# Optimization experiments

Measured on AMD Instinct MI355X. Metric: run time of the kernel, lower is better.

## Reference

```python
import jax, jax.numpy as jnp
import numpy as np

H = 16  # n_heads

def _split_heads(x, n_heads):
    B, S, Dm = x.shape
    return x.reshape(B, S, n_heads, Dm // n_heads).transpose(0, 2, 1, 3)  # [B,H,S,D]

def _matmul_prefix_sum(x, y, z):
    """Faithful, efficient form of the TF matmul_prefix_sum.
    TF builds yz[s] = y[s] (x) z[s] outer products, cumsums over s, then
    contracts with x[t]/ (t+1).  That equals a causal-masked bilinear form:
      out[t, j] = (1/(t+1)) * sum_{s<=t} (x[t]. y[s]) * z[s, j]
    so we compute (x y^T * tril / idx) @ z without the 5D intermediate.
    """
    S = x.shape[2]
    idx = jnp.arange(1, S + 1, dtype=x.dtype)[:, None]        # position 1..S
    mask = jnp.tril(jnp.ones((S, S), dtype=x.dtype))
    scores = jnp.einsum('bhtd,bhsd->bhts', x, y) * (mask / idx)
    return jnp.einsum('bhts,bhsj->bhtj', scores, z)

def setup_inputs() -> dict:
    key = jax.random.key(0)
    ks = jax.random.split(key, 12)
    B, S, Dm = 2, 1024, 1024
    f32 = jnp.float32
    rn = lambda k, shp: jax.random.normal(k, shp, dtype=f32)
    w_scale = f32(1.0 / np.sqrt(Dm))
    return {
        'v': rn(ks[0], (B, S, Dm)),
        'k': rn(ks[1], (B, S, Dm)),
        'q': rn(ks[2], (B, S, Dm)),
        'p': rn(ks[3], (B, S, Dm)),
        'wq_k': rn(ks[4], (Dm, Dm)) * w_scale, 'wq_b': jnp.zeros((Dm,), f32),
        'wk_k': rn(ks[5], (Dm, Dm)) * w_scale, 'wk_b': jnp.zeros((Dm,), f32),
        'wv_k': rn(ks[6], (Dm, Dm)) * w_scale, 'wv_b': jnp.zeros((Dm,), f32),
        'wc_k': rn(ks[7], (Dm, Dm)) * w_scale, 'wc_b': jnp.zeros((Dm,), f32),
    }

def reference(v, k, q, p, wq_k, wq_b, wk_k, wk_b, wv_k, wv_b, wc_k, wc_b):
    B, S, Dm = q.shape
    D = Dm // H
    norm_d = 1.0 / jnp.sqrt(jnp.asarray(D, q.dtype))
    ph = _split_heads(p, H)                                    # [B,H,S,D]
    qh = _split_heads((q @ wq_k + wq_b) * norm_d, H)
    kh = _split_heads(k @ wk_k + wk_b, H)
    vh = _split_heads(v @ wv_k + wv_b, H)
    # elu(p q^T)+1 then transpose -> indexed [B,H,t(query),s(p-position)]
    attn_pack = jax.nn.elu(jnp.einsum('bhtd,bhsd->bhts', qh, ph)) + 1.0
    attn_unpack = _matmul_prefix_sum(qh, kh, attn_pack)        # [B,H,S,S]
    attn_unpack = jax.nn.softmax(attn_unpack, axis=-1)
    attn_out = _matmul_prefix_sum(attn_unpack, attn_pack, vh)  # [B,H,S,D]
    attn_out = attn_out.transpose(0, 2, 1, 3).reshape(B, S, Dm)
    return attn_out @ wc_k + wc_b
```

## Files before the change

kernel.cpp:

```cpp
#include <hip/hip_runtime.h>

#define DEVI static __device__ __forceinline__

using s16x8 = __attribute__((ext_vector_type(8))) short;
using f32x4 = __attribute__((ext_vector_type(4))) float;
using u32x4 = __attribute__((ext_vector_type(4))) unsigned int;

static constexpr int H  = 16;
static constexpr int S  = 1024;
static constexpr int DM = 1024;
static constexpr int NB = 2;
static constexpr int BS = NB * S;
static constexpr long SS  = (long)S * S;
static constexpr long HSS = (long)H * SS;
static constexpr long SDM = (long)S * DM;

DEVI unsigned short f2bf(float f) {
    union { float f; unsigned u; } c; c.f = f;
    c.u += 0x7FFFu + ((c.u >> 16) & 1u);
    return (unsigned short)(c.u >> 16);
}
DEVI float bf2f(unsigned short v) {
    union { unsigned u; float f; } c; c.u = ((unsigned)v) << 16;
    return c.f;
}

DEVI void gload16(const unsigned short* g, unsigned short* l) {
    __builtin_amdgcn_global_load_lds(
        (const __attribute__((address_space(1))) unsigned int*)g,
        (__attribute__((address_space(3))) unsigned int*)l, 16, 0, 0);
}

enum { EPI_BFB = 0, EPI_VTB, EPI_PACK, EPI_PACK2, EPI_MASK, EPI_BF, EPI_OUT };

template<int EPI, bool CK, bool CS, bool SWZ, bool REVY>
__global__ __launch_bounds__(256)
void gemmS(const unsigned short* __restrict__ Aall, long a_sb, long a_sh, int lda,
           const unsigned short* __restrict__ Ball, long b_sb, long b_sh, int ldb,
           void* __restrict__ Oall, void* __restrict__ O2, long o_sb, long o_sh, int ldo,
           const float* __restrict__ bias, int bstride, int K, int NV)
{
    int bx, by, bz;
    if (SWZ) {
        const int L = (int)blockIdx.x + ((int)blockIdx.y << 3) + ((int)blockIdx.z << 6);
        const int g = L & 7, r = L >> 3;
        bz = g + ((r >> 6) << 3);
        bx = r & 7;
        by = 7 - ((r >> 3) & 7);
    } else {
        bx = blockIdx.x;
        by = REVY ? (int)gridDim.y - 1 - (int)blockIdx.y : (int)blockIdx.y;
        bz = blockIdx.z;
    }
    const int m0 = by * 128, n0 = bx * 128;
    if (CS && n0 > m0 + 127) return;
    const int zb = bz >> 4, zh = bz & 15;
    const unsigned short* Ap = Aall + (long)zb * a_sb + (long)zh * a_sh;
    const unsigned short* Bp = Ball + (long)zb * b_sb + (long)zh * b_sh;
    const float* bi = bias + (long)zh * bstride;

    __shared__ alignas(16) unsigned short lA[128 * 64];
    __shared__ alignas(16) unsigned short lB[128 * 64];

    const int tid = threadIdx.x, w = tid >> 6, lane = tid & 63;
    const int lr = lane & 15, lg = lane >> 4;
    const int wm = (w >> 1) << 6, wn = (w & 1) << 6;

    const unsigned short* gA[4]; const unsigned short* gB[4]; int lo[4];
#pragma unroll
    for (int i = 0; i < 4; ++i) {
        const int q = (i * 4 + w) * 64 + lane, row = q >> 3, slot = q & 7;
        const int gs = (slot ^ (row & 7)) * 8;
        gA[i] = Ap + (long)(m0 + row) * lda + gs;
        int rb = n0 + row; if (rb >= NV) rb = NV - 1;
        gB[i] = Bp + (long)rb * ldb + gs;
        lo[i] = (i * 4 + w) * 512;
    }

    int abase[4], axor[4], bbase[4], bxor[4];
#pragma unroll
    for (int f = 0; f < 4; ++f) {
        const int ra = wm + f * 16 + lr;
        abase[f] = ra * 64; axor[f] = (ra & 7) * 8;
        const int rb = wn + f * 16 + lr;
        bbase[f] = rb * 64; bxor[f] = (rb & 7) * 8;
    }

    f32x4 acc[4][4] = {};
    const int Keff = CK ? ((K < m0 + 128) ? K : m0 + 128) : K;

    for (int k0 = 0; k0 < Keff; k0 += 64) {
#pragma unroll
        for (int i = 0; i < 4; ++i) {
            gload16(gA[i] + k0, &lA[lo[i]]);
            gload16(gB[i] + k0, &lB[lo[i]]);
        }
        __syncthreads();
#pragma unroll
        for (int kk = 0; kk < 64; kk += 32) {
            s16x8 af[4], bv[4];
#pragma unroll
            for (int f = 0; f < 4; ++f) {
                af[f] = *reinterpret_cast<const s16x8*>(&lA[abase[f] + ((kk + 8 * lg) ^ axor[f])]);
                bv[f] = *reinterpret_cast<const s16x8*>(&lB[bbase[f] + ((kk + 8 * lg) ^ bxor[f])]);
            }
#pragma unroll
            for (int fm = 0; fm < 4; ++fm)
#pragma unroll
                for (int fn = 0; fn < 4; ++fn)
                    acc[fm][fn] = __builtin_amdgcn_mfma_f32_16x16x32_bf16(af[fm], bv[fn], acc[fm][fn], 0, 0, 0);
        }
        __syncthreads();
    }

    const long obase = (long)zb * o_sb + (long)zh * o_sh;
#pragma unroll
    for (int fm = 0; fm < 4; ++fm)
#pragma unroll
        for (int fn = 0; fn < 4; ++fn) {
            const int t0 = m0 + wm + fm * 16 + lg * 4;
            const int gn = n0 + wn + fn * 16 + lr;
            if (gn >= NV) continue;
            if constexpr (EPI == EPI_PACK2) {
                ushort4 pt;
                unsigned short* o1 = (unsigned short*)Oall;
                unsigned short* o2 = (unsigned short*)O2;
#pragma unroll
                for (int r = 0; r < 4; ++r) {
                    float vv = acc[fm][fn][r];
                    vv = vv > 0.f ? vv + 1.f : __expf(vv);
                    const unsigned short b = f2bf(vv);
                    o1[obase + (long)(t0 + r) * ldo + gn] = b;
                    ((unsigned short*)&pt)[r] = b;
                }
                *reinterpret_cast<ushort4*>(&o2[obase + (long)gn * ldo + t0]) = pt;
            } else {
#pragma unroll
                for (int r = 0; r < 4; ++r) {
                    const int gm = t0 + r;
                    float vv = acc[fm][fn][r];
                    const long o = obase + (long)gm * ldo + gn;
                    if constexpr (EPI == EPI_BFB) {
                        ((unsigned short*)Oall)[o] = f2bf(vv + bi[gn]);
                    } else if constexpr (EPI == EPI_VTB) {
                        ((unsigned short*)Oall)[o] = f2bf(vv + bi[gm]);
                    } else if constexpr (EPI == EPI_PACK) {
                        vv = vv > 0.f ? vv + 1.f : __expf(vv);
                        ((unsigned short*)Oall)[o] = f2bf(vv);
                    } else if constexpr (EPI == EPI_MASK) {
                        vv = (gn <= gm) ? vv / (float)(gm + 1) : 0.f;
                        ((unsigned short*)Oall)[o] = f2bf(vv);
                    } else if constexpr (EPI == EPI_BF) {
                        ((unsigned short*)Oall)[o] = f2bf(vv);
                    } else {
                        ((float*)Oall)[o] = vv + bi[gn];
                    }
                }
            }
        }
}

template<int TM, int TN, int EPI, bool CK, bool CS, bool REVY>
__global__ __launch_bounds__((TM/64)*(TN/64)*64)
void gemmT(const unsigned short* __restrict__ Aall, long a_sb, long a_sh, int lda,
           const unsigned short* __restrict__ Ball, long b_sb, long b_sh, int ldb,
           void* __restrict__ Oall, long o_sb, long o_sh, int ldo,
           const float* __restrict__ bias, int bstride, int K, int NV)
{
    constexpr int WN = TN / 64, WM = TM / 64, NWV = WM * WN, NTHR = NWV * 64;
    constexpr int IA = (TM * 8) / NTHR, IB = (TN * 8) / NTHR;

    const int bx = blockIdx.x;
    const int by = REVY ? (int)gridDim.y - 1 - (int)blockIdx.y : (int)blockIdx.y;
    const int bz = blockIdx.z;
    const int m0 = by * TM, n0 = bx * TN;
    if (CS && n0 > m0 + TM - 1) return;
    const int zb = bz >> 4, zh = bz & 15;
    const unsigned short* Ap = Aall + (long)zb * a_sb + (long)zh * a_sh;
    const unsigned short* Bp = Ball + (long)zb * b_sb + (long)zh * b_sh;
    const float* bi = bias + (long)zh * bstride;

    __shared__ alignas(16) unsigned short lA[TM * 64];
    __shared__ alignas(16) unsigned short lB[TN * 64];

    const int tid = threadIdx.x, w = tid >> 6, lane = tid & 63;
    const int lr = lane & 15, lg = lane >> 4;
    const int wm = (w / WN) * 64, wn = (w % WN) * 64;

    const unsigned short* gA[IA]; int loA[IA];
    const unsigned short* gB[IB]; int loB[IB];
#pragma unroll
    for (int i = 0; i < IA; ++i) {
        const int q = i * NTHR + tid, row = q >> 3, slot = q & 7;
        gA[i]  = Ap + (long)(m0 + row) * lda + ((slot ^ (row & 7)) * 8);
        loA[i] = (i * NWV + w) * 512;
    }
#pragma unroll
    for (int i = 0; i < IB; ++i) {
        const int q = i * NTHR + tid, row = q >> 3, slot = q & 7;
        int rb = n0 + row; if (rb >= NV) rb = NV - 1;
        gB[i]  = Bp + (long)rb * ldb + ((slot ^ (row & 7)) * 8);
        loB[i] = (i * NWV + w) * 512;
    }

    int abase[4], axor[4], bbase[4], bxor[4];
#pragma unroll
    for (int f = 0; f < 4; ++f) {
        const int ra = wm + f * 16 + lr;
        abase[f] = ra * 64; axor[f] = (ra & 7) * 8;
        const int rb = wn + f * 16 + lr;
        bbase[f] = rb * 64; bxor[f] = (rb & 7) * 8;
    }

    f32x4 acc[4][4] = {};
    const int Keff = CK ? ((K < m0 + TM) ? K : m0 + TM) : K;

    for (int k0 = 0; k0 < Keff; k0 += 64) {
#pragma unroll
        for (int i = 0; i < IA; ++i) gload16(gA[i] + k0, &lA[loA[i]]);
#pragma unroll
        for (int i = 0; i < IB; ++i) gload16(gB[i] + k0, &lB[loB[i]]);
        __syncthreads();
#pragma unroll
        for (int kk = 0; kk < 64; kk += 32) {
            s16x8 af[4], bv[4];
#pragma unroll
            for (int f = 0; f < 4; ++f) {
                af[f] = *reinterpret_cast<const s16x8*>(&lA[abase[f] + ((kk + 8 * lg) ^ axor[f])]);
                bv[f] = *reinterpret_cast<const s16x8*>(&lB[bbase[f] + ((kk + 8 * lg) ^ bxor[f])]);
            }
#pragma unroll
            for (int fm = 0; fm < 4; ++fm)
#pragma unroll
                for (int fn = 0; fn < 4; ++fn)
                    acc[fm][fn] = __builtin_amdgcn_mfma_f32_16x16x32_bf16(af[fm], bv[fn], acc[fm][fn], 0, 0, 0);
        }
        __syncthreads();
    }

    const long obase = (long)zb * o_sb + (long)zh * o_sh;
#pragma unroll
    for (int fm = 0; fm < 4; ++fm)
#pragma unroll
        for (int fn = 0; fn < 4; ++fn) {
            const int t0 = m0 + wm + fm * 16 + lg * 4;
            const int gn = n0 + wn + fn * 16 + lr;
            if (gn >= NV) continue;
#pragma unroll
            for (int r = 0; r < 4; ++r) {
                const int gm = t0 + r;
                float vv = acc[fm][fn][r];
                const long o = obase + (long)gm * ldo + gn;
                if constexpr (EPI == EPI_BFB) {
                    ((unsigned short*)Oall)[o] = f2bf(vv + bi[gn]);
                } else if constexpr (EPI == EPI_VTB) {
                    ((unsigned short*)Oall)[o] = f2bf(vv + bi[gm]);
                } else if constexpr (EPI == EPI_PACK) {
                    vv = vv > 0.f ? vv + 1.f : __expf(vv);
                    ((unsigned short*)Oall)[o] = f2bf(vv);
                } else if constexpr (EPI == EPI_MASK) {
                    vv = (gn <= gm) ? vv / (float)(gm + 1) : 0.f;
                    ((unsigned short*)Oall)[o] = f2bf(vv);
                } else if constexpr (EPI == EPI_BF) {
                    ((unsigned short*)Oall)[o] = f2bf(vv);
                } else {
                    ((float*)Oall)[o] = vv + bi[gn];
                }
            }
        }
}

__global__ __launch_bounds__(256)
void packsqk(const unsigned short* __restrict__ qh,
             const unsigned short* __restrict__ pbf,
             const unsigned short* __restrict__ kh,
             unsigned short* __restrict__ P, unsigned short* __restrict__ PT,
             unsigned short* __restrict__ SQ)
{
    const int L = (int)blockIdx.x + ((int)blockIdx.y << 3) + ((int)blockIdx.z << 6);
    const int g = L & 7, r = L >> 3;
    const int bzz = g + ((r >> 6) << 3);
    const int bx = r & 7, by = 7 - ((r >> 3) & 7);
    const int job = bzz >> 5, zz = bzz & 31;
    const int m0 = by * 128, n0 = bx * 128;
    if (job && n0 > m0 + 127) return;
    const int zb = zz >> 4, zh = zz & 15;
    const unsigned short* Ap = qh + (long)zb * SDM + zh * 64;
    const unsigned short* Bp = (job ? kh : pbf) + (long)zb * SDM + zh * 64;

    __shared__ alignas(16) unsigned short lA[128 * 64];
    __shared__ alignas(16) unsigned short lB[128 * 64];

    const int tid = threadIdx.x, w = tid >> 6, lane = tid & 63;
    const int lr = lane & 15, lg = lane >> 4;
    const int wm = (w >> 1) << 6, wn = (w & 1) << 6;

#pragma unroll
    for (int i = 0; i < 4; ++i) {
        const int q = i * 256 + tid, row = q >> 3, slot = q & 7;
        const int gs = (slot ^ (row & 7)) * 8;
        gload16(Ap + (long)(m0 + row) * DM + gs, &lA[(i * 4 + w) * 512]);
        gload16(Bp + (long)(n0 + row) * DM + gs, &lB[(i * 4 + w) * 512]);
    }
    __syncthreads();

    f32x4 acc[4][4] = {};
#pragma unroll
    for (int kk = 0; kk < 64; kk += 32) {
        s16x8 af[4], bv[4];
#pragma unroll
        for (int f = 0; f < 4; ++f) {
            const int ra = wm + f * 16 + lr;
            af[f] = *reinterpret_cast<const s16x8*>(&lA[ra * 64 + ((kk + 8 * lg) ^ ((ra & 7) * 8))]);
            const int rb = wn + f * 16 + lr;
            bv[f] = *reinterpret_cast<const s16x8*>(&lB[rb * 64 + ((kk + 8 * lg) ^ ((rb & 7) * 8))]);
        }
#pragma unroll
        for (int fm = 0; fm < 4; ++fm)
#pragma unroll
            for (int fn = 0; fn < 4; ++fn)
                acc[fm][fn] = __builtin_amdgcn_mfma_f32_16x16x32_bf16(af[fm], bv[fn], acc[fm][fn], 0, 0, 0);
    }

    const long obase = (long)zz * SS;
#pragma unroll
    for (int fm = 0; fm < 4; ++fm)
#pragma unroll
        for (int fn = 0; fn < 4; ++fn) {
            const int t0 = m0 + wm + fm * 16 + lg * 4;
            const int gn = n0 + wn + fn * 16 + lr;
            if (job == 0) {
                ushort4 pt;
#pragma unroll
                for (int rr = 0; rr < 4; ++rr) {
                    float vv = acc[fm][fn][rr];
                    vv = vv > 0.f ? vv + 1.f : __expf(vv);
                    const unsigned short b = f2bf(vv);
                    P[obase + (long)(t0 + rr) * S + gn] = b;
                    ((unsigned short*)&pt)[rr] = b;
                }
                *reinterpret_cast<ushort4*>(&PT[obase + (long)gn * S + t0]) = pt;
            } else {
#pragma unroll
                for (int rr = 0; rr < 4; ++rr) {
                    const int gm = t0 + rr;
                    float vv = acc[fm][fn][rr];
                    vv = (gn <= gm) ? vv / (float)(gm + 1) : 0.f;
                    SQ[obase + (long)gm * S + gn] = f2bf(vv);
                }
            }
        }
}

__global__ __launch_bounds__(256)
void softmax_rows(const unsigned short* __restrict__ in, unsigned short* __restrict__ out)
{
    const int w = threadIdx.x >> 6, lane = threadIdx.x & 63;
    const long row = (long)blockIdx.x * 4 + w;
    const u32x4* r4 = reinterpret_cast<const u32x4*>(in + row * S);
    u32x4 a = r4[lane * 2], b = r4[lane * 2 + 1];
    float v[16];
#pragma unroll
    for (int i = 0; i < 4; ++i) {
        v[2*i]     = bf2f((unsigned short)(a[i] & 0xFFFF));
        v[2*i+1]   = bf2f((unsigned short)(a[i] >> 16));
        v[8+2*i]   = bf2f((unsigned short)(b[i] & 0xFFFF));
        v[8+2*i+1] = bf2f((unsigned short)(b[i] >> 16));
    }
    float mx = v[0];
#pragma unroll
    for (int i = 1; i < 16; ++i) mx = fmaxf(mx, v[i]);
#pragma unroll
    for (int off = 32; off; off >>= 1) mx = fmaxf(mx, __shfl_xor(mx, off));
    float e[16], s = 0.f;
#pragma unroll
    for (int i = 0; i < 16; ++i) { e[i] = __expf(v[i] - mx); s += e[i]; }
#pragma unroll
    for (int off = 32; off; off >>= 1) s += __shfl_xor(s, off);
    const float inv = 1.f / s;
    u32x4 oa, ob;
#pragma unroll
    for (int i = 0; i < 4; ++i) {
        oa[i] = (unsigned)f2bf(e[2*i]   * inv) | ((unsigned)f2bf(e[2*i+1]   * inv) << 16);
        ob[i] = (unsigned)f2bf(e[8+2*i] * inv) | ((unsigned)f2bf(e[8+2*i+1] * inv) << 16);
    }
    u32x4* o4 = reinterpret_cast<u32x4*>(out + row * S);
    o4[lane * 2] = oa; o4[lane * 2 + 1] = ob;
}

__global__ __launch_bounds__(256)
void prep(const float* __restrict__ q_in, const float* __restrict__ k_in,
          const float* __restrict__ v_in, const float* __restrict__ p_in,
          const float* __restrict__ wq, const float* __restrict__ wk,
          const float* __restrict__ wv, const float* __restrict__ wc,
          const float* __restrict__ wqb, const float* __restrict__ wkb,
          unsigned short* __restrict__ qbf, unsigned short* __restrict__ wqT,
          float* __restrict__ bq2, int n4)
{
    const int z = blockIdx.z, bx = blockIdx.x, tid = threadIdx.x;
    if (z < 4) {
        const int i = bx * 256 + tid;
        if (i >= n4) return;
        const float* s = (z == 0) ? q_in : (z == 1) ? k_in : (z == 2) ? v_in : p_in;
        float4 x = reinterpret_cast<const float4*>(s)[i];
        ushort4 o; o.x = f2bf(x.x); o.y = f2bf(x.y); o.z = f2bf(x.z); o.w = f2bf(x.w);
        reinterpret_cast<ushort4*>(qbf + (size_t)z * n4 * 4)[i] = o;
    } else if (z < 8) {
        if (bx >= 256) return;
        __shared__ unsigned short t[64][72];
        const int zz = z - 4;
        const float* src = (zz == 0) ? wq : (zz == 1) ? wk : (zz == 2) ? wv : wc;
        const float scale = (zz == 0) ? 0.125f : 1.0f;
        unsigned short* dst = wqT + (size_t)zz * DM * DM;
        const int r0 = (bx >> 4) * 64, c0 = (bx & 15) * 64;
        const int lrow = tid >> 2, lseg = (tid & 3) << 4;
        const float4* g4 = reinterpret_cast<const float4*>(src + (long)(r0 + lrow) * DM + c0 + lseg);
        alignas(16) unsigned short tmp[16];
#pragma unroll
        for (int qq = 0; qq < 4; ++qq) {
            float4 x = g4[qq];
            tmp[4*qq+0] = f2bf(x.x * scale); tmp[4*qq+1] = f2bf(x.y * scale);
            tmp[4*qq+2] = f2bf(x.z * scale); tmp[4*qq+3] = f2bf(x.w * scale);
        }
#pragma unroll
        for (int j = 0; j < 16; ++j) t[lrow][lseg + j] = tmp[j];
        __syncthreads();
#pragma unroll
        for (int j = 0; j < 16; ++j) tmp[j] = t[lseg + j][lrow];
        unsigned short* d = dst + (long)(c0 + lrow) * DM + r0 + lseg;
        *reinterpret_cast<u32x4*>(d)     = *reinterpret_cast<const u32x4*>(tmp);
        *reinterpret_cast<u32x4*>(d + 8) = *reinterpret_cast<const u32x4*>(tmp + 8);
    } else {
        if (bx >= 4) return;
        const int i = bx * 256 + tid;
        if (i < DM) { bq2[i] = wqb[i] * 0.125f; bq2[DM + i] = wkb[i]; }
    }
}

extern "C" void kernel_launch(void* const* d_in, const int* in_sizes, int n_in,
                              void* d_out, int out_size, void* d_ws, size_t ws_size,
                              hipStream_t stream)
{
    (void)in_sizes; (void)n_in; (void)out_size;
    const float* v_in = (const float*)d_in[0];
    const float* k_in = (const float*)d_in[1];
    const float* q_in = (const float*)d_in[2];
    const float* p_in = (const float*)d_in[3];
    const float* wq   = (const float*)d_in[4];
    const float* wqb  = (const float*)d_in[5];
    const float* wk   = (const float*)d_in[6];
    const float* wkb  = (const float*)d_in[7];
    const float* wvw  = (const float*)d_in[8];
    const float* wvb  = (const float*)d_in[9];
    const float* wc   = (const float*)d_in[10];
    const float* wcb  = (const float*)d_in[11];
    float* out = (float*)d_out;

    char* ws = (char*)d_ws;
    size_t off = 0;
    auto take = [&](size_t n) { char* p = ws + off; off += (n + 255) & ~(size_t)255; return p; };
    unsigned short* qbf = (unsigned short*)take((size_t)BS * DM * 2);
    unsigned short* kbf = (unsigned short*)take((size_t)BS * DM * 2);
    unsigned short* vbf = (unsigned short*)take((size_t)BS * DM * 2);
    unsigned short* pbf = (unsigned short*)take((size_t)BS * DM * 2);
    unsigned short* wqT = (unsigned short*)take((size_t)DM * DM * 2);
    unsigned short* wkT = (unsigned short*)take((size_t)DM * DM * 2);
    unsigned short* wvT = (unsigned short*)take((size_t)DM * DM * 2);
    unsigned short* wcT = (unsigned short*)take((size_t)DM * DM * 2);
    float*          bq2 = (float*)take((size_t)2 * DM * 4);
    unsigned short* qh  = (unsigned short*)take((size_t)BS * DM * 2);
    unsigned short* kh  = (unsigned short*)take((size_t)BS * DM * 2);
    unsigned short* vhT = (unsigned short*)take((size_t)BS * DM * 2);
    unsigned short* ao  = (unsigned short*)take((size_t)BS * DM * 2);
    const size_t ssz = (size_t)NB * HSS * 2;
    unsigned short* B1 = (unsigned short*)take(ssz);
    unsigned short* B2 = (unsigned short*)take(ssz);
    unsigned short* B3 = (unsigned short*)take(ssz);
    const bool dual = (ws_size >= off + ssz);
    unsigned short* B4 = dual ? (unsigned short*)take(ssz) : nullptr;
    (void)kbf; (void)wkT;

    const int n4 = BS * DM / 4;
    const dim3 b256(256), b128(128);

    prep<<<dim3(n4 / 256, 1, 9), b256, 0, stream>>>(
        q_in, k_in, v_in, p_in, wq, wk, wvw, wc, wqb, wkb, qbf, wqT, bq2, n4);

    gemmT<64,128,EPI_BFB,false,false,false><<<dim3(8, 32, 2), b128, 0, stream>>>(
        qbf, 0, (long)BS*DM, DM,  wqT, 0, (long)DM*DM, DM,  qh, 0, (long)BS*DM, DM,
        bq2, DM, DM, DM);
    gemmT<64,128,EPI_VTB,false,false,false><<<dim3(8, 16, 2), b128, 0, stream>>>(
        wvT, 0, 0, DM,  vbf, 0, SDM, DM,  vhT, 0, (long)DM*S, S,
        wvb, 0, DM, S);

    unsigned short *pbuf, *ptbuf, *sqkbuf, *lbuf, *smbuf, *s2buf;
    if (dual) {
        packsqk<<<dim3(8, 8, 64), b256, 0, stream>>>(qh, pbf, kh, B1, B2, B3);
        pbuf = B1; ptbuf = B2; sqkbuf = B3; lbuf = B4; smbuf = B3; s2buf = B2;
    } else {
        gemmT<128,128,EPI_PACK,false,false,false><<<dim3(8, 8, 32), b256, 0, stream>>>(
            pbf, SDM, 64, DM,  qh, SDM, 64, DM,  B1, HSS, SS, S,  wvb, 0, 64, S);
        gemmT<128,128,EPI_MASK,false,true,true><<<dim3(8, 8, 32), b256, 0, stream>>>(
            qh, SDM, 64, DM,  kh, SDM, 64, DM,  B2, HSS, SS, S,  wvb, 0, 64, S);
        ptbuf = B1; sqkbuf = B2; lbuf = B3; smbuf = B2; pbuf = B1; s2buf = B3;
    }
    gemmS<EPI_BF,true,false,true,false><<<dim3(8, 8, 32), b256, 0, stream>>>(
        sqkbuf, HSS, SS, S,  ptbuf, HSS, SS, S,  lbuf, nullptr, HSS, SS, S,  wvb, 0, S, S);
    softmax_rows<<<dim3(NB*H*S/4), b256, 0, stream>>>(lbuf, smbuf);
    if (!dual) {
        gemmT<128,128,EPI_PACK,false,false,false><<<dim3(8, 8, 32), b256, 0, stream>>>(
            qh, SDM, 64, DM,  pbf, SDM, 64, DM,  B1, HSS, SS, S,  wvb, 0, 64, S);
    }
    gemmS<EPI_MASK,false,true,true,false><<<dim3(8, 8, 32), b256, 0, stream>>>(
        smbuf, HSS, SS, S,  pbuf, HSS, SS, S,  s2buf, nullptr, HSS, SS, S,  wvb, 0, S, S);
    gemmT<128,64,EPI_BF,true,false,true><<<dim3(1, 8, 32), b128, 0, stream>>>(
        s2buf, HSS, SS, S,  vhT, (long)DM*S, (long)64*S, S,  ao, SDM, 64, DM,
        wvb, 0, S, 64);
    gemmT<64,128,EPI_OUT,false,false,false><<<dim3(8, 32, 1), b128, 0, stream>>>(
        ao, 0, 0, DM,  wcT, 0, 0, DM,  out, 0, 0, DM,  wcb, 0, DM, DM);
}
```

Before: 319.5 us.

## Fuse softmax into adjacent GEMMs via exp epilogue and deferred row normalization

Removes the separate softmax kernel. The first prefix-sum GEMM now writes exp(score) in bf16 and atomically accumulates per-row sums, and the second GEMM folds the 1/(sum*(t+1)) scaling into its masked epilogue. This drops one full read/write pass over the [B,H,S,S] buffer. In exchange it adds a memset plus atomics, and it skips the max subtraction, which risks overflow if scores are large. The loads in the gemmT global-to-LDS loop are also interleaved.

Measured after the change: 315.6 us. About the same (-1.2%).

```diff
diff --git a/kernel.cpp b/kernel.cpp
--- a/kernel.cpp
+++ b/kernel.cpp
@@ -31,33 +31,21 @@
         (__attribute__((address_space(3))) unsigned int*)l, 16, 0, 0);
 }
 
-enum { EPI_BFB = 0, EPI_VTB, EPI_PACK, EPI_PACK2, EPI_MASK, EPI_BF, EPI_OUT };
-
-template<int EPI, bool CK, bool CS, bool SWZ, bool REVY>
+enum { EPI_BFB = 0, EPI_VTB, EPI_PACK, EPI_MASK, EPI_BF, EPI_OUT };
+
 __global__ __launch_bounds__(256)
-void gemmS(const unsigned short* __restrict__ Aall, long a_sb, long a_sh, int lda,
-           const unsigned short* __restrict__ Ball, long b_sb, long b_sh, int ldb,
-           void* __restrict__ Oall, void* __restrict__ O2, long o_sb, long o_sh, int ldo,
-           const float* __restrict__ bias, int bstride, int K, int NV)
+void gemmE(const unsigned short* __restrict__ Aall,
+           const unsigned short* __restrict__ Ball,
+           unsigned short* __restrict__ Oall, float* __restrict__ sums)
 {
-    int bx, by, bz;
-    if (SWZ) {
-        const int L = (int)blockIdx.x + ((int)blockIdx.y << 3) + ((int)blockIdx.z << 6);
-        const int g = L & 7, r = L >> 3;
-        bz = g + ((r >> 6) << 3);
-        bx = r & 7;
-        by = 7 - ((r >> 3) & 7);
-    } else {
-        bx = blockIdx.x;
-        by = REVY ? (int)gridDim.y - 1 - (int)blockIdx.y : (int)blockIdx.y;
-        bz = blockIdx.z;
-    }
+    const int L = (int)blockIdx.x + ((int)blockIdx.y << 3) + ((int)blockIdx.z << 6);
+    const int g = L & 7, r = L >> 3;
+    const int bz = g + ((r >> 6) << 3);
+    const int bx = r & 7;
+    const int by = 7 - ((r >> 3) & 7);
     const int m0 = by * 128, n0 = bx * 128;
-    if (CS && n0 > m0 + 127) return;
-    const int zb = bz >> 4, zh = bz & 15;
-    const unsigned short* Ap = Aall + (long)zb * a_sb + (long)zh * a_sh;
-    const unsigned short* Bp = Ball + (long)zb * b_sb + (long)zh * b_sh;
-    const float* bi = bias + (long)zh * bstride;
+    const unsigned short* Ap = Aall + (long)bz * SS;
+    const unsigned short* Bp = Ball + (long)bz * SS;
 
     __shared__ alignas(16) unsigned short lA[128 * 64];
     __shared__ alignas(16) unsigned short lB[128 * 64];
@@ -71,9 +59,8 @@
     for (int i = 0; i < 4; ++i) {
         const int q = (i * 4 + w) * 64 + lane, row = q >> 3, slot = q & 7;
         const int gs = (slot ^ (row & 7)) * 8;
-        gA[i] = Ap + (long)(m0 + row) * lda + gs;
-        int rb = n0 + row; if (rb >= NV) rb = NV - 1;
-        gB[i] = Bp + (long)rb * ldb + gs;
+        gA[i] = Ap + (long)(m0 + row) * S + gs;
+        gB[i] = Bp + (long)(n0 + row) * S + gs;
         lo[i] = (i * 4 + w) * 512;
     }
 
@@ -87,7 +74,7 @@
     }
 
     f32x4 acc[4][4] = {};
-    const int Keff = CK ? ((K < m0 + 128) ? K : m0 + 128) : K;
+    const int Keff = m0 + 128;
 
     for (int k0 = 0; k0 < Keff; k0 += 64) {
 #pragma unroll
@@ -113,51 +100,117 @@
         __syncthreads();
     }
 
-    const long obase = (long)zb * o_sb + (long)zh * o_sh;
-#pragma unroll
-    for (int fm = 0; fm < 4; ++fm)
+    const long obase = (long)bz * SS;
+#pragma unroll
+    for (int fm = 0; fm < 4; ++fm) {
+        const int t0 = m0 + wm + fm * 16 + lg * 4;
+        float es[4] = {0.f, 0.f, 0.f, 0.f};
 #pragma unroll
         for (int fn = 0; fn < 4; ++fn) {
-            const int t0 = m0 + wm + fm * 16 + lg * 4;
             const int gn = n0 + wn + fn * 16 + lr;
-            if (gn >= NV) continue;
-            if constexpr (EPI == EPI_PACK2) {
-                ushort4 pt;
-                unsigned short* o1 = (unsigned short*)Oall;
-                unsigned short* o2 = (unsigned short*)O2;
-#pragma unroll
-                for (int r = 0; r < 4; ++r) {
-                    float vv = acc[fm][fn][r];
-                    vv = vv > 0.f ? vv + 1.f : __expf(vv);
-                    const unsigned short b = f2bf(vv);
-                    o1[obase + (long)(t0 + r) * ldo + gn] = b;
-                    ((unsigned short*)&pt)[r] = b;
-                }
-                *reinterpret_cast<ushort4*>(&o2[obase + (long)gn * ldo + t0]) = pt;
-            } else {
-#pragma unroll
-                for (int r = 0; r < 4; ++r) {
-                    const int gm = t0 + r;
-                    float vv = acc[fm][fn][r];
-                    const long o = obase + (long)gm * ldo + gn;
-                    if constexpr (EPI == EPI_BFB) {
-                        ((unsigned short*)Oall)[o] = f2bf(vv + bi[gn]);
-                    } else if constexpr (EPI == EPI_VTB) {
-                        ((unsigned short*)Oall)[o] = f2bf(vv + bi[gm]);
-                    } else if constexpr (EPI == EPI_PACK) {
-                        vv = vv > 0.f ? vv + 1.f : __expf(vv);
-                        ((unsigned short*)Oall)[o] = f2bf(vv);
-                    } else if constexpr (EPI == EPI_MASK) {
-                        vv = (gn <= gm) ? vv / (float)(gm + 1) : 0.f;
-                        ((unsigned short*)Oall)[o] = f2bf(vv);
-                    } else if constexpr (EPI == EPI_BF) {
-                        ((unsigned short*)Oall)[o] = f2bf(vv);
-                    } else {
-                        ((float*)Oall)[o] = vv + bi[gn];
-                    }
-                }
-            }
-        }
+#pragma unroll
+            for (int rr = 0; rr < 4; ++rr) {
+                const float e = __expf(acc[fm][fn][rr]);
+                Oall[obase + (long)(t0 + rr) * S + gn] = f2bf(e);
+                es[rr] += e;
+            }
+        }
+#pragma unroll
+        for (int rr = 0; rr < 4; ++rr) {
+            float s = es[rr];
+            s += __shfl_xor(s, 1); s += __shfl_xor(s, 2);
+            s += __shfl_xor(s, 4); s += __shfl_xor(s, 8);
+            if (lr == 0) atomicAdd(&sums[(long)bz * S + t0 + rr], s);
+        }
+    }
+}
+
+__global__ __launch_bounds__(256)
+void gemmZ(const unsigned short* __restrict__ Aall,
+           const unsigned short* __restrict__ Ball,
+           unsigned short* __restrict__ Oall, const float* __restrict__ sums)
+{
+    const int L = (int)blockIdx.x + ((int)blockIdx.y << 3) + ((int)blockIdx.z << 6);
+    const int g = L & 7, r = L >> 3;
+    const int bz = g + ((r >> 6) << 3);
+    const int bx = r & 7;
+    const int by = 7 - ((r >> 3) & 7);
+    const int m0 = by * 128, n0 = bx * 128;
+    if (n0 > m0 + 127) return;
+    const unsigned short* Ap = Aall + (long)bz * SS;
+    const unsigned short* Bp = Ball + (long)bz * SS;
+
+    __shared__ alignas(16) unsigned short lA[128 * 64];
+    __shared__ alignas(16) unsigned short lB[128 * 64];
+
+    const int tid = threadIdx.x, w = tid >> 6, lane = tid & 63;
+    const int lr = lane & 15, lg = lane >> 4;
+    const int wm = (w >> 1) << 6, wn = (w & 1) << 6;
+
+    const unsigned short* gA[4]; const unsigned short* gB[4]; int lo[4];
+#pragma unroll
+    for (int i = 0; i < 4; ++i) {
+        const int q = (i * 4 + w) * 64 + lane, row = q >> 3, slot = q & 7;
+        const int gs = (slot ^ (row & 7)) * 8;
+        gA[i] = Ap + (long)(m0 + row) * S + gs;
+        gB[i] = Bp + (long)(n0 + row) * S + gs;
+        lo[i] = (i * 4 + w) * 512;
+    }
+
+    int abase[4], axor[4], bbase[4], bxor[4];
+#pragma unroll
+    for (int f = 0; f < 4; ++f) {
+        const int ra = wm + f * 16 + lr;
+        abase[f] = ra * 64; axor[f] = (ra & 7) * 8;
+        const int rb = wn + f * 16 + lr;
+        bbase[f] = rb * 64; bxor[f] = (rb & 7) * 8;
+    }
+
+    f32x4 acc[4][4] = {};
+
+    for (int k0 = 0; k0 < S; k0 += 64) {
+#pragma unroll
+        for (int i = 0; i < 4; ++i) {
+            gload16(gA[i] + k0, &lA[lo[i]]);
+            gload16(gB[i] + k0, &lB[lo[i]]);
+        }
+        __syncthreads();
+#pragma unroll
+        for (int kk = 0; kk < 64; kk += 32) {
+            s16x8 af[4], bv[4];
+#pragma unroll
+            for (int f = 0; f < 4; ++f) {
+                af[f] = *reinterpret_cast<const s16x8*>(&lA[abase[f] + ((kk + 8 * lg) ^ axor[f])]);
+                bv[f] = *reinterpret_cast<const s16x8*>(&lB[bbase[f] + ((kk + 8 * lg) ^ bxor[f])]);
+            }
+#pragma unroll
+            for (int fm = 0; fm < 4; ++fm)
+#pragma unroll
+                for (int fn = 0; fn < 4; ++fn)
+                    acc[fm][fn] = __builtin_amdgcn_mfma_f32_16x16x32_bf16(af[fm], bv[fn], acc[fm][fn], 0, 0, 0);
+        }
+        __syncthreads();
+    }
+
+    const long obase = (long)bz * SS;
+#pragma unroll
+    for (int fm = 0; fm < 4; ++fm) {
+        const int t0 = m0 + wm + fm * 16 + lg * 4;
+        float rec[4];
+#pragma unroll
+        for (int rr = 0; rr < 4; ++rr)
+            rec[rr] = 1.f / (sums[(long)bz * S + t0 + rr] * (float)(t0 + rr + 1));
+#pragma unroll
+        for (int fn = 0; fn < 4; ++fn) {
+            const int gn = n0 + wn + fn * 16 + lr;
+#pragma unroll
+            for (int rr = 0; rr < 4; ++rr) {
+                const int gm = t0 + rr;
+                const float vv = (gn <= gm) ? acc[fm][fn][rr] * rec[rr] : 0.f;
+                Oall[obase + (long)gm * S + gn] = f2bf(vv);
+            }
+        }
+    }
 }
 
 template<int TM, int TN, int EPI, bool CK, bool CS, bool REVY>
@@ -169,6 +222,7 @@
 {
     constexpr int WN = TN / 64, WM = TM / 64, NWV = WM * WN, NTHR = NWV * 64;
     constexpr int IA = (TM * 8) / NTHR, IB = (TN * 8) / NTHR;
+    constexpr int IMX = IA > IB ? IA : IB;
 
     const int bx = blockIdx.x;
     const int by = REVY ? (int)gridDim.y - 1 - (int)blockIdx.y : (int)blockIdx.y;
@@ -217,9 +271,10 @@
 
     for (int k0 = 0; k0 < Keff; k0 += 64) {
 #pragma unroll
-        for (int i = 0; i < IA; ++i) gload16(gA[i] + k0, &lA[loA[i]]);
-#pragma unroll
-        for (int i = 0; i < IB; ++i) gload16(gB[i] + k0, &lB[loB[i]]);
+        for (int i = 0; i < IMX; ++i) {
+            if (i < IA) gload16(gA[i] + k0, &lA[loA[i]]);
+            if (i < IB) gload16(gB[i] + k0, &lB[loB[i]]);
+        }
         __syncthreads();
 #pragma unroll
         for (int kk = 0; kk < 64; kk += 32) {
@@ -350,42 +405,6 @@
                 }
             }
         }
-}
-
-__global__ __launch_bounds__(256)
-void softmax_rows(const unsigned short* __restrict__ in, unsigned short* __restrict__ out)
-{
-    const int w = threadIdx.x >> 6, lane = threadIdx.x & 63;
-    const long row = (long)blockIdx.x * 4 + w;
-    const u32x4* r4 = reinterpret_cast<const u32x4*>(in + row * S);
-    u32x4 a = r4[lane * 2], b = r4[lane * 2 + 1];
-    float v[16];
-#pragma unroll
-    for (int i = 0; i < 4; ++i) {
-        v[2*i]     = bf2f((unsigned short)(a[i] & 0xFFFF));
-        v[2*i+1]   = bf2f((unsigned short)(a[i] >> 16));
-        v[8+2*i]   = bf2f((unsigned short)(b[i] & 0xFFFF));
-        v[8+2*i+1] = bf2f((unsigned short)(b[i] >> 16));
-    }
-    float mx = v[0];
-#pragma unroll
-    for (int i = 1; i < 16; ++i) mx = fmaxf(mx, v[i]);
-#pragma unroll
-    for (int off = 32; off; off >>= 1) mx = fmaxf(mx, __shfl_xor(mx, off));
-    float e[16], s = 0.f;
-#pragma unroll
-    for (int i = 0; i < 16; ++i) { e[i] = __expf(v[i] - mx); s += e[i]; }
-#pragma unroll
-    for (int off = 32; off; off >>= 1) s += __shfl_xor(s, off);
-    const float inv = 1.f / s;
-    u32x4 oa, ob;
-#pragma unroll
-    for (int i = 0; i < 4; ++i) {
-        oa[i] = (unsigned)f2bf(e[2*i]   * inv) | ((unsigned)f2bf(e[2*i+1]   * inv) << 16);
-        ob[i] = (unsigned)f2bf(e[8+2*i] * inv) | ((unsigned)f2bf(e[8+2*i+1] * inv) << 16);
-    }
-    u32x4* o4 = reinterpret_cast<u32x4*>(out + row * S);
-    o4[lane * 2] = oa; o4[lane * 2 + 1] = ob;
 }
 
 __global__ __launch_bounds__(256)
@@ -468,6 +487,7 @@
     unsigned short* wvT = (unsigned short*)take((size_t)DM * DM * 2);
     unsigned short* wcT = (unsigned short*)take((size_t)DM * DM * 2);
     float*          bq2 = (float*)take((size_t)2 * DM * 4);
+    float*          sums= (float*)take((size_t)NB * H * S * 4);
     unsigned short* qh  = (unsigned short*)take((size_t)BS * DM * 2);
     unsigned short* kh  = (unsigned short*)take((size_t)BS * DM * 2);
     unsigned short* vhT = (unsigned short*)take((size_t)BS * DM * 2);
@@ -483,6 +503,7 @@
     const int n4 = BS * DM / 4;
     const dim3 b256(256), b128(128);
 
+    hipMemsetAsync(sums, 0, (size_t)NB * H * S * 4, stream);
     prep<<<dim3(n4 / 256, 1, 9), b256, 0, stream>>>(
         q_in, k_in, v_in, p_in, wq, wk, wvw, wc, wqb, wkb, qbf, wqT, bq2, n4);
 
@@ -493,26 +514,23 @@
         wvT, 0, 0, DM,  vbf, 0, SDM, DM,  vhT, 0, (long)DM*S, S,
         wvb, 0, DM, S);
 
-    unsigned short *pbuf, *ptbuf, *sqkbuf, *lbuf, *smbuf, *s2buf;
+    unsigned short *pbuf, *ptbuf, *sqkbuf, *ebuf, *s2buf;
     if (dual) {
         packsqk<<<dim3(8, 8, 64), b256, 0, stream>>>(qh, pbf, kh, B1, B2, B3);
-        pbuf = B1; ptbuf = B2; sqkbuf = B3; lbuf = B4; smbuf = B3; s2buf = B2;
+        pbuf = B1; ptbuf = B2; sqkbuf = B3; ebuf = B4; s2buf = B3;
     } else {
         gemmT<128,128,EPI_PACK,false,false,false><<<dim3(8, 8, 32), b256, 0, stream>>>(
             pbf, SDM, 64, DM,  qh, SDM, 64, DM,  B1, HSS, SS, S,  wvb, 0, 64, S);
         gemmT<128,128,EPI_MASK,false,true,true><<<dim3(8, 8, 32), b256, 0, stream>>>(
             qh, SDM, 64, DM,  kh, SDM, 64, DM,  B2, HSS, SS, S,  wvb, 0, 64, S);
-        ptbuf = B1; sqkbuf = B2; lbuf = B3; smbuf = B2; pbuf = B1; s2buf = B3;
-    }
-    gemmS<EPI_BF,true,false,true,false><<<dim3(8, 8, 32), b256, 0, stream>>>(
-        sqkbuf, HSS, SS, S,  ptbuf, HSS, SS, S,  lbuf, nullptr, HSS, SS, S,  wvb, 0, S, S);
-    softmax_rows<<<dim3(NB*H*S/4), b256, 0, stream>>>(lbuf, smbuf);
+        ptbuf = B1; sqkbuf = B2; ebuf = B3; pbuf = B1; s2buf = B2;
+    }
+    gemmE<<<dim3(8, 8, 32), b256, 0, stream>>>(sqkbuf, ptbuf, ebuf, sums);
     if (!dual) {
         gemmT<128,128,EPI_PACK,false,false,false><<<dim3(8, 8, 32), b256, 0, stream>>>(
             qh, SDM, 64, DM,  pbf, SDM, 64, DM,  B1, HSS, SS, S,  wvb, 0, 64, S);
     }
-    gemmS<EPI_MASK,false,true,true,false><<<dim3(8, 8, 32), b256, 0, stream>>>(
-        smbuf, HSS, SS, S,  pbuf, HSS, SS, S,  s2buf, nullptr, HSS, SS, S,  wvb, 0, S, S);
+    gemmZ<<<dim3(8, 8, 32), b256, 0, stream>>>(ebuf, pbuf, s2buf, sums);
     gemmT<128,64,EPI_BF,true,false,true><<<dim3(1, 8, 32), b128, 0, stream>>>(
         s2buf, HSS, SS, S,  vhT, (long)DM*S, (long)64*S, S,  ao, SDM, 64, DM,
         wvb, 0, S, 64);
```
